# Optimization experiments

Measured on AMD Instinct MI355X. Metric: run time of the kernel, lower is better.

Reference implementation:

```python
import jax, jax.numpy as jnp
import numpy as np

N_NODES = 100000
N_EDGES = 1600000
IN_F = 128
N_HEADS = 8
HEAD_D = 8  # n_hidden // n_heads = 64 // 8
NEG_SLOPE = 0.2


def setup_inputs() -> dict:
    key = jax.random.key(0)
    k1, k2, k3, k4, k5 = jax.random.split(key, 5)
    vert = jax.random.normal(k1, (N_NODES, IN_F), dtype=jnp.float32)
    edge = jax.random.randint(k2, (2, N_EDGES), 0, N_NODES, dtype=jnp.int64)
    scale_w = 1.0 / np.sqrt(IN_F)
    W = jax.random.normal(k3, (IN_F, N_HEADS, HEAD_D), dtype=jnp.float32) * scale_w
    scale_a = 1.0 / np.sqrt(HEAD_D)
    a_src = jax.random.normal(k4, (N_HEADS, HEAD_D), dtype=jnp.float32) * scale_a
    a_dst = jax.random.normal(k5, (N_HEADS, HEAD_D), dtype=jnp.float32) * scale_a
    return {"vert": vert, "edge": edge, "W": W, "a_src": a_src, "a_dst": a_dst}


def reference(vert, edge, W, a_src, a_dst):
    # Per-head linear projection: [N, H, D]
    g = jnp.einsum('nf,fhd->nhd', vert, W)
    src, dst = edge[0], edge[1]
    # Decomposed attention logits: e_ij = LeakyReLU(a_src.g_i + a_dst.g_j)
    e_s = jnp.sum(g * a_src[None], axis=-1)  # [N, H]
    e_d = jnp.sum(g * a_dst[None], axis=-1)  # [N, H]
    scores = jax.nn.leaky_relu(e_s[src] + e_d[dst], NEG_SLOPE)  # [E, H]
    # Segment softmax over incoming edges of each destination node
    m = jax.ops.segment_max(scores, dst, num_segments=N_NODES)  # [N, H]
    m = jnp.where(jnp.isneginf(m), 0.0, m)
    ex = jnp.exp(scores - m[dst])  # [E, H]
    denom = jax.ops.segment_sum(ex, dst, num_segments=N_NODES)  # [N, H]
    alpha = ex / jnp.maximum(denom[dst], 1e-16)  # [E, H]
    # Weighted message aggregation: scatter-add alpha * g[src] into dst
    msg = alpha[:, :, None] * g[src]  # [E, H, D]
    agg = jax.ops.segment_sum(msg, dst, num_segments=N_NODES)  # [N, H, D]
    out = agg.reshape(N_NODES, N_HEADS * HEAD_D)  # concat heads
    # GAT_DE trailing ELU (dropout=0.0 -> identity)
    return jax.nn.elu(out)
```

## Files before the change

### kernel.cpp

```cpp
#include <hip/hip_runtime.h>
#include <hip/hip_bf16.h>
#include <hip/hip_fp16.h>
#include <math.h>

#define N_NODES 100000
#define N_EDGES 1600000
#define IN_F    128
#define NH      8
#define HD      8
#define HID     64
#define NEG_SLOPE 0.2f

#define BSH   5
#define BSZ   32
#define NBK   3125
#define NCB   196
#define CSTR  9216
#define BCAP  832
#define NBPJ  782
#define NPB   160
#define EPB   10000
#define GSTR  16

typedef short bf16x8 __attribute__((ext_vector_type(8)));
typedef float f32x4  __attribute__((ext_vector_type(4)));

static __device__ __forceinline__ unsigned short f2bf(float x) {
    __hip_bfloat16 h = __float2bfloat16(x);
    return *(unsigned short*)&h;
}

__global__ __launch_bounds__(256) void prep_kernel(
    const float* __restrict__ W, const float* __restrict__ a_src,
    const float* __restrict__ a_dst, unsigned short* __restrict__ Bg,
    int* __restrict__ gcnt)
{
    const int tid = threadIdx.x;
    for (int i = blockIdx.x * 256 + tid; i < NCB * GSTR; i += 16 * 256) gcnt[i] = 0;
    if (blockIdx.x != 0) return;

    __shared__ __align__(16) unsigned short bl[10240];
    for (int idx = tid; idx < 128 * 16; idx += 256) {
        const int f = idx >> 4, cq = idx & 15;
        const float4 w = *(const float4*)(W + f * 64 + cq * 4);
        const int kc = f >> 5, q = (f >> 3) & 3, j = f & 7;
        const float wf[4] = {w.x, w.y, w.z, w.w};
        #pragma unroll
        for (int i = 0; i < 4; ++i) {
            const int col = cq * 4 + i;
            bl[(col >> 4) * 2048 + kc * 512 + q * 128 + (col & 15) * 8 + j] = f2bf(wf[i]);
        }
    }
    for (int idx = tid; idx < 128 * 8; idx += 256) {
        const int f = idx >> 3, h = idx & 7;
        const float4 wa = *(const float4*)(W + f * 64 + h * 8);
        const float4 wb = *(const float4*)(W + f * 64 + h * 8 + 4);
        const float4 sa = *(const float4*)(a_src + h * 8);
        const float4 sb = *(const float4*)(a_src + h * 8 + 4);
        const float4 da = *(const float4*)(a_dst + h * 8);
        const float4 db = *(const float4*)(a_dst + h * 8 + 4);
        float esv = fmaf(wa.x, sa.x, fmaf(wa.y, sa.y, fmaf(wa.z, sa.z,
                    fmaf(wa.w, sa.w, fmaf(wb.x, sb.x, fmaf(wb.y, sb.y,
                    fmaf(wb.z, sb.z, wb.w * sb.w)))))));
        float edv = fmaf(wa.x, da.x, fmaf(wa.y, da.y, fmaf(wa.z, da.z,
                    fmaf(wa.w, da.w, fmaf(wb.x, db.x, fmaf(wb.y, db.y,
                    fmaf(wb.z, db.z, wb.w * db.w)))))));
        const int kc = f >> 5, q = (f >> 3) & 3, j = f & 7;
        bl[4 * 2048 + kc * 512 + q * 128 + h * 8 + j]       = f2bf(esv);
        bl[4 * 2048 + kc * 512 + q * 128 + (8 + h) * 8 + j] = f2bf(edv);
    }
    __syncthreads();
    for (int idx = tid; idx < 1280; idx += 256)
        ((uint4*)Bg)[idx] = ((const uint4*)bl)[idx];
}

__global__ __launch_bounds__(512) void fused_pp_kernel(
    const float* __restrict__ vert, const unsigned short* __restrict__ Bg,
    __hip_bfloat16* __restrict__ gb, float* __restrict__ es, float* __restrict__ ed,
    const int* __restrict__ edge, int* __restrict__ gcnt,
    unsigned int* __restrict__ packed)
{
    __shared__ __align__(16) char smem[28672];
    const int tid = threadIdx.x;

    if (blockIdx.x < NBPJ) {
        unsigned short* b_lds = (unsigned short*)smem;
        const int nbeg = blockIdx.x * 128;
        const int lane = tid & 63, wv = tid >> 6;
        const int mn   = lane & 15, quad = lane >> 4;

        for (int idx = tid; idx < 1280; idx += 512)
            *(uint4*)(smem + idx * 16) = ((const uint4*)Bg)[idx];

        const int row = nbeg + wv * 16 + mn;
        bf16x8 afr[4];
        #pragma unroll
        for (int kc = 0; kc < 4; ++kc) {
            float4 p = make_float4(0.f, 0.f, 0.f, 0.f);
            float4 q4 = make_float4(0.f, 0.f, 0.f, 0.f);
            if (row < N_NODES) {
                const float* rp = vert + (size_t)row * IN_F + kc * 32 + quad * 8;
                p  = *(const float4*)rp;
                q4 = *(const float4*)(rp + 4);
            }
            bf16x8 a;
            a[0] = (short)f2bf(p.x);  a[1] = (short)f2bf(p.y);
            a[2] = (short)f2bf(p.z);  a[3] = (short)f2bf(p.w);
            a[4] = (short)f2bf(q4.x); a[5] = (short)f2bf(q4.y);
            a[6] = (short)f2bf(q4.z); a[7] = (short)f2bf(q4.w);
            afr[kc] = a;
        }
        __syncthreads();

        const unsigned short* bbase = b_lds + quad * 128 + mn * 8;
        f32x4 acc[5];
        #pragma unroll
        for (int c = 0; c < 5; ++c) acc[c] = (f32x4){0.f, 0.f, 0.f, 0.f};
        #pragma unroll
        for (int kc = 0; kc < 4; ++kc) {
            #pragma unroll
            for (int c = 0; c < 5; ++c) {
                const bf16x8 bfr = *(const bf16x8*)(bbase + c * 2048 + kc * 512);
                acc[c] = __builtin_amdgcn_mfma_f32_16x16x32_bf16(afr[kc], bfr, acc[c], 0, 0, 0);
            }
        }
        __syncthreads();

        unsigned short* gl = (unsigned short*)smem + wv * 1152;
        float* lesd = (float*)(smem + 18432) + wv * 320;
        #pragma unroll
        for (int c = 0; c < 4; ++c)
            #pragma unroll
            for (int r = 0; r < 4; ++r)
                gl[(quad * 4 + r) * 72 + c * 16 + mn] = f2bf(acc[c][r]);
        {
            float* dst = (mn < 8) ? (lesd + mn) : (lesd + 160 + (mn - 8));
            #pragma unroll
            for (int r = 0; r < 4; ++r) dst[(quad * 4 + r) * 10] = acc[4][r];
        }
        __syncthreads();
        {
            const int row2 = lane >> 2, part = lane & 3;
            const int node = nbeg + wv * 16 + row2;
            if (node < N_NODES) {
                const uint4* sp = (const uint4*)(gl + row2 * 72 + part * 16);
                *(uint4*)((unsigned short*)gb + (size_t)node * HID + part * 16) = sp[0];
                *(uint4*)((unsigned short*)gb + (size_t)node * HID + part * 16 + 8) = sp[1];
            }
        }
        {
            const int nl = lane >> 2, h2 = (lane & 3) * 2;
            const int node = nbeg + wv * 16 + nl;
            if (node < N_NODES) {
                *(float2*)(es + node * NH + h2) = *(const float2*)(lesd + nl * 10 + h2);
                *(float2*)(ed + node * NH + h2) = *(const float2*)(lesd + 160 + nl * 10 + h2);
            }
        }
    } else {
        int* lh    = (int*)smem;
        int* lbase = (int*)(smem + 1024);
        const int pb = blockIdx.x - NBPJ;

        if (tid < NCB) lh[tid] = 0;
        __syncthreads();
        const int4* src4 = (const int4*)(edge + pb * EPB);
        const int4* dst4 = (const int4*)(edge + N_EDGES + pb * EPB);
        for (int t = tid; t < EPB / 4; t += 512) {
            const int4 d = dst4[t];
            atomicAdd(&lh[d.x >> 9], 1);
            atomicAdd(&lh[d.y >> 9], 1);
            atomicAdd(&lh[d.z >> 9], 1);
            atomicAdd(&lh[d.w >> 9], 1);
        }
        __syncthreads();
        if (tid < NCB) {
            const int c = lh[tid];
            lbase[tid] = c ? (tid * CSTR + atomicAdd(&gcnt[tid * GSTR], c)) : 0;
            lh[tid] = 0;
        }
        __syncthreads();
        for (int t = tid; t < EPB / 4; t += 512) {
            const int4 s = src4[t];
            const int4 d = dst4[t];
            int bk, pos;
            bk = d.x >> 9; pos = min(lbase[bk] + atomicAdd(&lh[bk], 1), NCB * CSTR - 1);
            packed[pos] = ((unsigned)s.x << 9) | (unsigned)(d.x & 511);
            bk = d.y >> 9; pos = min(lbase[bk] + atomicAdd(&lh[bk], 1), NCB * CSTR - 1);
            packed[pos] = ((unsigned)s.y << 9) | (unsigned)(d.y & 511);
            bk = d.z >> 9; pos = min(lbase[bk] + atomicAdd(&lh[bk], 1), NCB * CSTR - 1);
            packed[pos] = ((unsigned)s.z << 9) | (unsigned)(d.z & 511);
            bk = d.w >> 9; pos = min(lbase[bk] + atomicAdd(&lh[bk], 1), NCB * CSTR - 1);
            packed[pos] = ((unsigned)s.w << 9) | (unsigned)(d.w & 511);
        }
    }
}

__global__ __launch_bounds__(512) void radixb_kernel(
    const int* __restrict__ gcnt, unsigned int* __restrict__ packed,
    int2* __restrict__ finfo)
{
    __shared__ unsigned int ebuf[CSTR];
    __shared__ unsigned int stage[CSTR];
    __shared__ int fh[16], fpre[16];
    const int tid = threadIdx.x;
    const int cb  = blockIdx.x;
    const int cnt = min(gcnt[cb * GSTR], CSTR);
    unsigned int* in = packed + (size_t)cb * CSTR;

    if (tid < 16) fh[tid] = 0;
    __syncthreads();
    for (int i = tid; i < cnt; i += 512) {
        const unsigned v = in[i];
        ebuf[i] = v;
        atomicAdd(&fh[(v >> 5) & 15], 1);
    }
    __syncthreads();
    if (tid == 0) {
        int s = 0;
        #pragma unroll
        for (int f = 0; f < 16; ++f) { fpre[f] = s; s += fh[f]; }
    }
    __syncthreads();
    if (tid < 16) fh[tid] = fpre[tid];
    __syncthreads();
    for (int i = tid; i < cnt; i += 512) {
        const unsigned v = ebuf[i];
        const int pos = atomicAdd(&fh[(v >> 5) & 15], 1);
        stage[pos] = ((v >> 9) << 7) | (v & 31);
    }
    __syncthreads();
    for (int i = tid; i < cnt; i += 512) in[i] = stage[i];
    if (tid < 16) {
        const int fg = cb * 16 + tid;
        if (fg < NBK)
            finfo[fg] = make_int2(cb * CSTR + fpre[tid], fh[tid] - fpre[tid]);
    }
}

__global__ __launch_bounds__(256) void p2agg_kernel(
    const int2* __restrict__ finfo, const unsigned int* __restrict__ packed,
    const unsigned short* __restrict__ gb, const float* __restrict__ es,
    const float* __restrict__ ed, float* __restrict__ out)
{
    __shared__ unsigned int ssrt[BCAP];
    __shared__ __align__(16) unsigned short pexp[BCAP * 8];
    __shared__ int ldeg[BSZ], loffs[BSZ];
    __shared__ __align__(16) float led[BSZ * NH];
    unsigned int* epk = (unsigned int*)pexp;

    const int tid  = threadIdx.x;
    const int b    = blockIdx.x;
    const int nbeg = b << BSH;
    const int2 fi  = finfo[b];
    const int ebase = fi.x;
    const int ecnt  = min(fi.y, BCAP);

    if (tid < BSZ) ldeg[tid] = 0;
    for (int i = tid; i < BSZ * NH; i += 256) led[i] = ed[nbeg * NH + i];
    __syncthreads();

    for (int i = tid; i < ecnt; i += 256) {
        const unsigned int p = packed[ebase + i];
        epk[i] = p;
        atomicAdd(&ldeg[p & (BSZ - 1)], 1);
    }
    __syncthreads();

    if (tid < BSZ) {
        int v = ldeg[tid];
        #pragma unroll
        for (int off = 1; off < BSZ; off <<= 1) {
            const int t = __shfl_up(v, off, 64);
            if (tid >= off) v += t;
        }
        loffs[tid] = v - ldeg[tid];
    }
    __syncthreads();

    for (int i = tid; i < ecnt; i += 256) {
        const unsigned int p = epk[i];
        const int pos = atomicAdd(&loffs[p & (BSZ - 1)], 1);
        ssrt[pos] = p;
    }
    __syncthreads();

    for (int i = tid; i < ecnt; i += 256) {
        const unsigned pw = ssrt[i];
        const int src = (int)(pw >> 7), dl = (int)(pw & (BSZ - 1));
        const float4 e0 = *(const float4*)(es + (size_t)src * NH);
        const float4 e1 = *(const float4*)(es + (size_t)src * NH + 4);
        const float4 l0 = *(const float4*)(led + dl * NH);
        const float4 l1 = *(const float4*)(led + dl * NH + 4);
        float s[8] = {e0.x + l0.x, e0.y + l0.y, e0.z + l0.z, e0.w + l0.w,
                      e1.x + l1.x, e1.y + l1.y, e1.z + l1.z, e1.w + l1.w};
        #pragma unroll
        for (int k = 0; k < 8; ++k)
            s[k] = __expf(fmaxf(s[k], s[k] * NEG_SLOPE));
        __half2 h01 = __floats2half2_rn(s[0], s[1]);
        __half2 h23 = __floats2half2_rn(s[2], s[3]);
        __half2 h45 = __floats2half2_rn(s[4], s[5]);
        __half2 h67 = __floats2half2_rn(s[6], s[7]);
        uint4 w;
        w.x = *(unsigned*)&h01; w.y = *(unsigned*)&h23;
        w.z = *(unsigned*)&h45; w.w = *(unsigned*)&h67;
        *(uint4*)(pexp + i * 8) = w;
    }
    __syncthreads();

    const int lane  = tid & 63;
    const int wv    = tid >> 6;
    const int c2    = lane & 31;
    const int khalf = lane >> 5;
    const int h     = c2 >> 2;
    const unsigned c2_4 = (unsigned)(c2 << 2);
    const char* gbase = (const char*)gb;

#define BULK_STEP(s, pw)                                                      \
    {                                                                         \
        const float pe = __half2float(                                        \
            *(const __half*)(pexp + ((i + 2 * (s) + khalf) << 3) + h));       \
        const unsigned voff = ((pw) & ~127u) | c2_4;                          \
        const unsigned gu = *(const unsigned*)(gbase + voff);                 \
        acc0 = fmaf(pe, __uint_as_float(gu << 16), acc0);                     \
        acc1 = fmaf(pe, __uint_as_float(gu & 0xFFFF0000u), acc1);             \
        l += pe;                                                              \
    }

    for (int n = wv; n < BSZ; n += 4) {
        const int end = loffs[n];
        const int beg = end - ldeg[n];
        float l = 0.f, acc0 = 0.f, acc1 = 0.f;
        int i = beg;
        for (; i + 8 <= end; i += 8) {
            const unsigned pw0 = ssrt[i + khalf];
            const unsigned pw1 = ssrt[i + 2 + khalf];
            const unsigned pw2 = ssrt[i + 4 + khalf];
            const unsigned pw3 = ssrt[i + 6 + khalf];
            BULK_STEP(0, pw0); BULK_STEP(1, pw1);
            BULK_STEP(2, pw2); BULK_STEP(3, pw3);
        }
        if (i < end) {
            #pragma unroll
            for (int s = 0; s < 4; ++s) {
                const int e  = i + 2 * s + khalf;
                const int ec = min(e, end - 1);
                const unsigned pw = ssrt[ec];
                float pe = __half2float(*(const __half*)(pexp + (ec << 3) + h));
                pe = (e < end) ? pe : 0.f;
                const unsigned voff = (pw & ~127u) | c2_4;
                const unsigned gu = *(const unsigned*)(gbase + voff);
                acc0 = fmaf(pe, __uint_as_float(gu << 16), acc0);
                acc1 = fmaf(pe, __uint_as_float(gu & 0xFFFF0000u), acc1);
                l += pe;
            }
        }
        l    += __shfl_xor(l, 32);
        acc0 += __shfl_xor(acc0, 32);
        acc1 += __shfl_xor(acc1, 32);
        const float rl = 1.f / fmaxf(l, 1e-16f);
        float o0 = acc0 * rl, o1 = acc1 * rl;
        o0 = (o0 > 0.f) ? o0 : (__expf(o0) - 1.f);
        o1 = (o1 > 0.f) ? o1 : (__expf(o1) - 1.f);
        const float ov = khalf ? o1 : o0;
        out[(size_t)(nbeg + n) * HID + c2 * 2 + khalf] = ov;
    }
#undef BULK_STEP
}

extern "C" void kernel_launch(void* const* d_in, const int* in_sizes, int n_in,
                              void* d_out, int out_size, void* d_ws, size_t ws_size,
                              hipStream_t stream)
{
    const float* vert  = (const float*)d_in[0];
    const int*   edge  = (const int*)  d_in[1];
    const float* W     = (const float*)d_in[2];
    const float* a_src = (const float*)d_in[3];
    const float* a_dst = (const float*)d_in[4];
    float* out = (float*)d_out;

    char* ws = (char*)d_ws;
    __hip_bfloat16* gb     = (__hip_bfloat16*)(ws);
    float*          es     = (float*)(ws + 12800000);
    float*          ed     = (float*)(ws + 16000000);
    unsigned int*   packed = (unsigned int*)(ws + 19200000);
    int*            gcnt   = (int*)(ws + 26425344);
    int2*           finfo  = (int2*)(ws + 26437888);
    unsigned short* Bg     = (unsigned short*)(ws + 26462896);

    prep_kernel<<<16, 256, 0, stream>>>(W, a_src, a_dst, Bg, gcnt);
    fused_pp_kernel<<<NBPJ + NPB, 512, 0, stream>>>(
        vert, Bg, gb, es, ed, edge, gcnt, packed);
    radixb_kernel<<<NCB, 512, 0, stream>>>(gcnt, packed, finfo);
    p2agg_kernel<<<NBK, 256, 0, stream>>>(finfo, packed, (const unsigned short*)gb, es, ed, out);
}
```

Before: 177.2 us.

## Sort edges fully by destination node in radix pass, drop per-block local sort

The radix kernel now histograms and scatters on the full 9-bit local destination index (512 bins with a wave-level prefix scan) instead of 16 block-level bins. It writes the sorted stream straight to global memory, skipping the shared staging buffer, and emits per-node offset/count records. The aggregation kernel reads these per-node ranges directly, which removes its LDS histogram, scan and second scatter pass. It also switches the gather to 16 lanes x 4 channels with 4 edges in flight per wave, using uint2 loads and float4 stores. Risks are more LDS atomic contention over 512 bins, scattered global writes in the radix pass, and an extra shuffle level in the reduction.

```diff
diff --git a/kernel.cpp b/kernel.cpp
--- a/kernel.cpp
+++ b/kernel.cpp
@@ -197,95 +197,90 @@
 
 __global__ __launch_bounds__(512) void radixb_kernel(
     const int* __restrict__ gcnt, unsigned int* __restrict__ packed,
-    int2* __restrict__ finfo)
+    int2* __restrict__ nodeinfo)
 {
     __shared__ unsigned int ebuf[CSTR];
-    __shared__ unsigned int stage[CSTR];
-    __shared__ int fh[16], fpre[16];
+    __shared__ int fh[512], fpre[512];
+    __shared__ int wsum[8];
     const int tid = threadIdx.x;
     const int cb  = blockIdx.x;
     const int cnt = min(gcnt[cb * GSTR], CSTR);
     unsigned int* in = packed + (size_t)cb * CSTR;
 
-    if (tid < 16) fh[tid] = 0;
+    fh[tid] = 0;
     __syncthreads();
     for (int i = tid; i < cnt; i += 512) {
         const unsigned v = in[i];
         ebuf[i] = v;
-        atomicAdd(&fh[(v >> 5) & 15], 1);
-    }
-    __syncthreads();
-    if (tid == 0) {
-        int s = 0;
-        #pragma unroll
-        for (int f = 0; f < 16; ++f) { fpre[f] = s; s += fh[f]; }
-    }
-    __syncthreads();
-    if (tid < 16) fh[tid] = fpre[tid];
+        atomicAdd(&fh[v & 511], 1);
+    }
+    __syncthreads();
+    {
+        const int lane = tid & 63, wv = tid >> 6;
+        const int v = fh[tid];
+        int s = v;
+        #pragma unroll
+        for (int off = 1; off < 64; off <<= 1) {
+            const int t = __shfl_up(s, off, 64);
+            if (lane >= off) s += t;
+        }
+        if (lane == 63) wsum[wv] = s;
+        __syncthreads();
+        if (tid < 8) {
+            const int w = wsum[tid];
+            int e = w;
+            #pragma unroll
+            for (int off = 1; off < 8; off <<= 1) {
+                const int t = __shfl_up(e, off, 64);
+                if (tid >= off) e += t;
+            }
+            wsum[tid] = e - w;
+        }
+        __syncthreads();
+        const int ex = s - v + wsum[wv];
+        fpre[tid] = ex;
+        fh[tid]   = ex;
+    }
     __syncthreads();
     for (int i = tid; i < cnt; i += 512) {
         const unsigned v = ebuf[i];
-        const int pos = atomicAdd(&fh[(v >> 5) & 15], 1);
-        stage[pos] = ((v >> 9) << 7) | (v & 31);
-    }
-    __syncthreads();
-    for (int i = tid; i < cnt; i += 512) in[i] = stage[i];
-    if (tid < 16) {
-        const int fg = cb * 16 + tid;
-        if (fg < NBK)
-            finfo[fg] = make_int2(cb * CSTR + fpre[tid], fh[tid] - fpre[tid]);
-    }
+        const int pos = atomicAdd(&fh[v & 511], 1);
+        in[pos] = ((v >> 9) << 7) | (v & 31);
+    }
+    __syncthreads();
+    const int node = cb * 512 + tid;
+    if (node < N_NODES)
+        nodeinfo[node] = make_int2(cb * CSTR + fpre[tid], fh[tid] - fpre[tid]);
 }
 
 __global__ __launch_bounds__(256) void p2agg_kernel(
-    const int2* __restrict__ finfo, const unsigned int* __restrict__ packed,
+    const int2* __restrict__ nodeinfo, const unsigned int* __restrict__ packed,
     const unsigned short* __restrict__ gb, const float* __restrict__ es,
     const float* __restrict__ ed, float* __restrict__ out)
 {
     __shared__ unsigned int ssrt[BCAP];
     __shared__ __align__(16) unsigned short pexp[BCAP * 8];
-    __shared__ int ldeg[BSZ], loffs[BSZ];
+    __shared__ int sbeg[BSZ + 1];
     __shared__ __align__(16) float led[BSZ * NH];
-    unsigned int* epk = (unsigned int*)pexp;
 
     const int tid  = threadIdx.x;
     const int b    = blockIdx.x;
     const int nbeg = b << BSH;
-    const int2 fi  = finfo[b];
-    const int ebase = fi.x;
-    const int ecnt  = min(fi.y, BCAP);
-
-    if (tid < BSZ) ldeg[tid] = 0;
+    const int ebase = nodeinfo[nbeg].x;
+
+    if (tid < BSZ) {
+        const int2 ni = nodeinfo[nbeg + tid];
+        sbeg[tid] = ni.x - ebase;
+        if (tid == BSZ - 1) sbeg[BSZ] = ni.x + ni.y - ebase;
+    }
     for (int i = tid; i < BSZ * NH; i += 256) led[i] = ed[nbeg * NH + i];
     __syncthreads();
 
+    const int ecnt = min(sbeg[BSZ], BCAP);
+
     for (int i = tid; i < ecnt; i += 256) {
-        const unsigned int p = packed[ebase + i];
-        epk[i] = p;
-        atomicAdd(&ldeg[p & (BSZ - 1)], 1);
-    }
-    __syncthreads();
-
-    if (tid < BSZ) {
-        int v = ldeg[tid];
-        #pragma unroll
-        for (int off = 1; off < BSZ; off <<= 1) {
-            const int t = __shfl_up(v, off, 64);
-            if (tid >= off) v += t;
-        }
-        loffs[tid] = v - ldeg[tid];
-    }
-    __syncthreads();
-
-    for (int i = tid; i < ecnt; i += 256) {
-        const unsigned int p = epk[i];
-        const int pos = atomicAdd(&loffs[p & (BSZ - 1)], 1);
-        ssrt[pos] = p;
-    }
-    __syncthreads();
-
-    for (int i = tid; i < ecnt; i += 256) {
-        const unsigned pw = ssrt[i];
+        const unsigned pw = packed[ebase + i];
+        ssrt[i] = pw;
         const int src = (int)(pw >> 7), dl = (int)(pw & (BSZ - 1));
         const float4 e0 = *(const float4*)(es + (size_t)src * NH);
         const float4 e1 = *(const float4*)(es + (size_t)src * NH + 4);
@@ -307,64 +302,65 @@
     }
     __syncthreads();
 
-    const int lane  = tid & 63;
-    const int wv    = tid >> 6;
-    const int c2    = lane & 31;
-    const int khalf = lane >> 5;
-    const int h     = c2 >> 2;
-    const unsigned c2_4 = (unsigned)(c2 << 2);
+    const int lane = tid & 63;
+    const int wv   = tid >> 6;
+    const int c4   = lane & 15;
+    const int eg   = lane >> 4;
+    const int h    = c4 >> 1;
+    const unsigned c4_8 = (unsigned)(c4 << 3);
     const char* gbase = (const char*)gb;
 
-#define BULK_STEP(s, pw)                                                      \
+#define GSTEP(B)                                                              \
     {                                                                         \
-        const float pe = __half2float(                                        \
-            *(const __half*)(pexp + ((i + 2 * (s) + khalf) << 3) + h));       \
-        const unsigned voff = ((pw) & ~127u) | c2_4;                          \
-        const unsigned gu = *(const unsigned*)(gbase + voff);                 \
-        acc0 = fmaf(pe, __uint_as_float(gu << 16), acc0);                     \
-        acc1 = fmaf(pe, __uint_as_float(gu & 0xFFFF0000u), acc1);             \
+        const int e = (B) + eg;                                               \
+        const unsigned pw = ssrt[e];                                          \
+        const float pe = __half2float(*(const __half*)(pexp + (e << 3) + h)); \
+        const unsigned voff = (pw & ~127u) | c4_8;                            \
+        const uint2 gu = *(const uint2*)(gbase + voff);                       \
+        a0 = fmaf(pe, __uint_as_float(gu.x << 16), a0);                       \
+        a1 = fmaf(pe, __uint_as_float(gu.x & 0xFFFF0000u), a1);               \
+        a2 = fmaf(pe, __uint_as_float(gu.y << 16), a2);                       \
+        a3 = fmaf(pe, __uint_as_float(gu.y & 0xFFFF0000u), a3);               \
         l += pe;                                                              \
     }
 
     for (int n = wv; n < BSZ; n += 4) {
-        const int end = loffs[n];
-        const int beg = end - ldeg[n];
-        float l = 0.f, acc0 = 0.f, acc1 = 0.f;
+        const int beg = min(sbeg[n], ecnt);
+        const int end = min(sbeg[n + 1], ecnt);
+        float l = 0.f, a0 = 0.f, a1 = 0.f, a2 = 0.f, a3 = 0.f;
         int i = beg;
-        for (; i + 8 <= end; i += 8) {
-            const unsigned pw0 = ssrt[i + khalf];
-            const unsigned pw1 = ssrt[i + 2 + khalf];
-            const unsigned pw2 = ssrt[i + 4 + khalf];
-            const unsigned pw3 = ssrt[i + 6 + khalf];
-            BULK_STEP(0, pw0); BULK_STEP(1, pw1);
-            BULK_STEP(2, pw2); BULK_STEP(3, pw3);
-        }
-        if (i < end) {
-            #pragma unroll
-            for (int s = 0; s < 4; ++s) {
-                const int e  = i + 2 * s + khalf;
-                const int ec = min(e, end - 1);
-                const unsigned pw = ssrt[ec];
-                float pe = __half2float(*(const __half*)(pexp + (ec << 3) + h));
-                pe = (e < end) ? pe : 0.f;
-                const unsigned voff = (pw & ~127u) | c2_4;
-                const unsigned gu = *(const unsigned*)(gbase + voff);
-                acc0 = fmaf(pe, __uint_as_float(gu << 16), acc0);
-                acc1 = fmaf(pe, __uint_as_float(gu & 0xFFFF0000u), acc1);
-                l += pe;
-            }
-        }
-        l    += __shfl_xor(l, 32);
-        acc0 += __shfl_xor(acc0, 32);
-        acc1 += __shfl_xor(acc1, 32);
-        const float rl = 1.f / fmaxf(l, 1e-16f);
-        float o0 = acc0 * rl, o1 = acc1 * rl;
-        o0 = (o0 > 0.f) ? o0 : (__expf(o0) - 1.f);
-        o1 = (o1 > 0.f) ? o1 : (__expf(o1) - 1.f);
-        const float ov = khalf ? o1 : o0;
-        out[(size_t)(nbeg + n) * HID + c2 * 2 + khalf] = ov;
-    }
-#undef BULK_STEP
+        for (; i + 8 <= end; i += 8) { GSTEP(i) GSTEP(i + 4) }
+        for (; i < end; i += 4) {
+            const int e  = i + eg;
+            const int ec = min(e, end - 1);
+            const unsigned pw = ssrt[ec];
+            float pe = __half2float(*(const __half*)(pexp + (ec << 3) + h));
+            pe = (e < end) ? pe : 0.f;
+            const unsigned voff = (pw & ~127u) | c4_8;
+            const uint2 gu = *(const uint2*)(gbase + voff);
+            a0 = fmaf(pe, __uint_as_float(gu.x << 16), a0);
+            a1 = fmaf(pe, __uint_as_float(gu.x & 0xFFFF0000u), a1);
+            a2 = fmaf(pe, __uint_as_float(gu.y << 16), a2);
+            a3 = fmaf(pe, __uint_as_float(gu.y & 0xFFFF0000u), a3);
+            l += pe;
+        }
+        l  += __shfl_xor(l, 16);  l  += __shfl_xor(l, 32);
+        a0 += __shfl_xor(a0, 16); a0 += __shfl_xor(a0, 32);
+        a1 += __shfl_xor(a1, 16); a1 += __shfl_xor(a1, 32);
+        a2 += __shfl_xor(a2, 16); a2 += __shfl_xor(a2, 32);
+        a3 += __shfl_xor(a3, 16); a3 += __shfl_xor(a3, 32);
+        if (eg == 0) {
+            const float rl = 1.f / fmaxf(l, 1e-16f);
+            float o0 = a0 * rl, o1 = a1 * rl, o2 = a2 * rl, o3 = a3 * rl;
+            o0 = (o0 > 0.f) ? o0 : (__expf(o0) - 1.f);
+            o1 = (o1 > 0.f) ? o1 : (__expf(o1) - 1.f);
+            o2 = (o2 > 0.f) ? o2 : (__expf(o2) - 1.f);
+            o3 = (o3 > 0.f) ? o3 : (__expf(o3) - 1.f);
+            *(float4*)(out + (size_t)(nbeg + n) * HID + c4 * 4) =
+                make_float4(o0, o1, o2, o3);
+        }
+    }
+#undef GSTEP
 }
 
 extern "C" void kernel_launch(void* const* d_in, const int* in_sizes, int n_in,
@@ -384,12 +380,12 @@
     float*          ed     = (float*)(ws + 16000000);
     unsigned int*   packed = (unsigned int*)(ws + 19200000);
     int*            gcnt   = (int*)(ws + 26425344);
-    int2*           finfo  = (int2*)(ws + 26437888);
-    unsigned short* Bg     = (unsigned short*)(ws + 26462896);
+    int2*           nodeinfo = (int2*)(ws + 26437888);
+    unsigned short* Bg     = (unsigned short*)(ws + 27237888);
 
     prep_kernel<<<16, 256, 0, stream>>>(W, a_src, a_dst, Bg, gcnt);
     fused_pp_kernel<<<NBPJ + NPB, 512, 0, stream>>>(
         vert, Bg, gb, es, ed, edge, gcnt, packed);
-    radixb_kernel<<<NCB, 512, 0, stream>>>(gcnt, packed, finfo);
-    p2agg_kernel<<<NBK, 256, 0, stream>>>(finfo, packed, (const unsigned short*)gb, es, ed, out);
-}
+    radixb_kernel<<<NCB, 512, 0, stream>>>(gcnt, packed, nodeinfo);
+    p2agg_kernel<<<NBK, 256, 0, stream>>>(nodeinfo, packed, (const unsigned short*)gb, es, ed, out);
+}
```

Measured after the change: 182.8 us. 1.03x slower.
